# Kernel tuning notes

Measured on AMD Instinct MI355X. Metric: run time of the kernel, lower is better.

The kernel has to match this reference:

```python
import jax, jax.numpy as jnp
import numpy as np

B, T, C = 2, 2048, 1024
N_HEAD = 16
HEAD_DIM = C // N_HEAD


def setup_inputs() -> dict:
    key = jax.random.key(0)
    k1, k2, k3 = jax.random.split(key, 3)
    x = jax.random.normal(k1, (B, T, C), dtype=jnp.float32)
    # weights stored as [in, out]; torch Linear computes x @ W.T with weight [out, in]
    W_qkv = jax.random.normal(k2, (C, 3 * C), dtype=jnp.float32) * (1.0 / np.sqrt(C))
    W_proj = jax.random.normal(k3, (C, C), dtype=jnp.float32) * (1.0 / np.sqrt(C))
    return {"x": x, "W_qkv": W_qkv, "W_proj": W_proj}


def reference(x, W_qkv, W_proj):
    Bb, Tt, Cc = x.shape
    qkv = x @ W_qkv                                # [B,T,3C]
    q, k, v = jnp.split(qkv, 3, axis=2)
    # [B,T,H,D] -> [B,H,T,D]
    q = q.reshape(Bb, Tt, N_HEAD, HEAD_DIM).transpose(0, 2, 1, 3)
    k = k.reshape(Bb, Tt, N_HEAD, HEAD_DIM).transpose(0, 2, 1, 3)
    v = v.reshape(Bb, Tt, N_HEAD, HEAD_DIM).transpose(0, 2, 1, 3)
    scale = 1.0 / np.sqrt(HEAD_DIM).astype(np.float32)
    att = jnp.einsum('bhqd,bhkd->bhqk', q, k) * scale   # [B,H,T,T]
    causal = jnp.tril(jnp.ones((Tt, Tt), dtype=bool))
    att = jnp.where(causal[None, None], att, -jnp.inf)
    att = jax.nn.softmax(att, axis=-1)
    y = jnp.einsum('bhqk,bhkd->bhqd', att, v)           # [B,H,T,D]
    y = y.transpose(0, 2, 1, 3).reshape(Bb, Tt, Cc)
    return y @ W_proj
```

## Files before the change

### kernel.cpp

```cpp
#include <hip/hip_runtime.h>
#include <hip/hip_bf16.h>
#include <math.h>


typedef __bf16 bf16_t;
typedef __bf16 bf16x4 __attribute__((ext_vector_type(4)));
typedef __bf16 bf16x8 __attribute__((ext_vector_type(8)));
typedef float  f32x4  __attribute__((ext_vector_type(4)));

#define MFMA16(a, b, c) __builtin_amdgcn_mfma_f32_16x16x32_bf16((a), (b), (c), 0, 0, 0)

#define Bn 2
#define Tn 2048
#define Cn 1024
#define Hn 16
#define Dn 64
#define C3 3072
#define Mn 4096
#define QKW 2048
#define NEG_BIG (-1e30f)
#define SCL2 0.18033688011112042f
#define M2   17.31234049066756f

__device__ __forceinline__ void gload_lds16(const void* g, void* l) {
    __builtin_amdgcn_global_load_lds(
        (const __attribute__((address_space(1))) unsigned int*)g,
        (__attribute__((address_space(3))) unsigned int*)l, 16, 0, 0);
}

__device__ __forceinline__ bf16x8 cat44(bf16x4 a, bf16x4 b) {
    bf16x8 r;
    r[0] = a[0]; r[1] = a[1]; r[2] = a[2]; r[3] = a[3];
    r[4] = b[0]; r[5] = b[1]; r[6] = b[2]; r[7] = b[3];
    return r;
}

__global__ __launch_bounds__(256) void transpose_cvt(const float* __restrict__ in,
                                                     bf16_t* __restrict__ out,
                                                     int K, int N) {
    __shared__ float tile[32][33];
    int n0 = blockIdx.x * 32, k0 = blockIdx.y * 32;
    int tx = threadIdx.x, ty = threadIdx.y;
#pragma unroll
    for (int i = 0; i < 32; i += 8)
        tile[ty + i][tx] = in[(size_t)(k0 + ty + i) * N + n0 + tx];
    __syncthreads();
#pragma unroll
    for (int i = 0; i < 32; i += 8)
        out[(size_t)(n0 + ty + i) * K + k0 + tx] = (bf16_t)tile[tx][ty + i];
}

__global__ __launch_bounds__(256) void cvt_bf16(const float* __restrict__ in,
                                                bf16_t* __restrict__ out) {
    size_t i = ((size_t)blockIdx.x * 256 + threadIdx.x) * 8;
    f32x4 a = *(const f32x4*)(in + i);
    f32x4 b = *(const f32x4*)(in + i + 4);
    bf16x8 r;
    r[0] = (bf16_t)a[0]; r[1] = (bf16_t)a[1]; r[2] = (bf16_t)a[2]; r[3] = (bf16_t)a[3];
    r[4] = (bf16_t)b[0]; r[5] = (bf16_t)b[1]; r[6] = (bf16_t)b[2]; r[7] = (bf16_t)b[3];
    *(bf16x8*)(out + i) = r;
}

template <typename AT, typename CT, int MODE>
__global__ __launch_bounds__(256) void gemm_m97(const AT* __restrict__ A, int lda,
                                                const bf16_t* __restrict__ BT,
                                                CT* __restrict__ Cout, int ldc, int Kd,
                                                bf16_t* __restrict__ qk,
                                                bf16_t* __restrict__ vT) {
    constexpr bool AF32 = (sizeof(AT) == 4);
    __shared__ AT     As[128 * 32];
    __shared__ bf16_t Bs[128 * 32];

    const int tid = threadIdx.x;
    const int w = tid >> 6, lane = tid & 63;
    const int l16 = lane & 15, quad = lane >> 4;
    const int wm = w & 1, wn = w >> 1;
    const int n0 = blockIdx.x * 128;
    const int m0 = blockIdx.y * 128;

    f32x4 zero = {0.f, 0.f, 0.f, 0.f};
    f32x4 acc[4][4];
#pragma unroll
    for (int mb = 0; mb < 4; mb++)
#pragma unroll
        for (int nb = 0; nb < 4; nb++) acc[mb][nb] = zero;

    for (int k = 0; k < Kd; k += 32) {
        __syncthreads();
        if (AF32) {
#pragma unroll
            for (int j = 0; j < 4; j++) {
                int seg = w * 4 + j;
                int r = seg * 8 + (lane >> 3);
                int cc = (lane & 7) ^ (r & 7);
                const float* g = (const float*)A + (size_t)(m0 + r) * lda + k + cc * 4;
                gload_lds16(g, (char*)As + seg * 1024);
            }
        } else {
#pragma unroll
            for (int j = 0; j < 2; j++) {
                int seg = w * 2 + j;
                int r = seg * 16 + (lane >> 2);
                int cc = (lane & 3) ^ (r & 3);
                const bf16_t* g = (const bf16_t*)A + (size_t)(m0 + r) * lda + k + cc * 8;
                gload_lds16(g, (char*)As + seg * 1024);
            }
        }
#pragma unroll
        for (int j = 0; j < 2; j++) {
            int seg = w * 2 + j;
            int r = seg * 16 + (lane >> 2);
            int cc = (lane & 3) ^ (r & 3);
            const bf16_t* g = BT + (size_t)(n0 + r) * Kd + k + cc * 8;
            gload_lds16(g, (char*)Bs + seg * 1024);
        }
        __syncthreads();

        bf16x8 af[4], bf[4];
#pragma unroll
        for (int mb = 0; mb < 4; mb++) {
            int r = wm * 64 + mb * 16 + l16;
            if (AF32) {
                f32x4 x0 = *(const f32x4*)((const char*)As + (r * 8 + ((quad * 2) ^ (r & 7))) * 16);
                f32x4 x1 = *(const f32x4*)((const char*)As + (r * 8 + ((quad * 2 + 1) ^ (r & 7))) * 16);
                bf16x8 t;
                t[0] = (bf16_t)x0[0]; t[1] = (bf16_t)x0[1]; t[2] = (bf16_t)x0[2]; t[3] = (bf16_t)x0[3];
                t[4] = (bf16_t)x1[0]; t[5] = (bf16_t)x1[1]; t[6] = (bf16_t)x1[2]; t[7] = (bf16_t)x1[3];
                af[mb] = t;
            } else {
                af[mb] = *(const bf16x8*)((const char*)As + (r * 4 + (quad ^ (r & 3))) * 16);
            }
        }
#pragma unroll
        for (int nb = 0; nb < 4; nb++) {
            int r = wn * 64 + nb * 16 + l16;
            bf[nb] = *(const bf16x8*)((const char*)Bs + (r * 4 + (quad ^ (r & 3))) * 16);
        }
#pragma unroll
        for (int mb = 0; mb < 4; mb++)
#pragma unroll
            for (int nb = 0; nb < 4; nb++)
                acc[mb][nb] = MFMA16(af[mb], bf[nb], acc[mb][nb]);
    }

#pragma unroll
    for (int mb = 0; mb < 4; mb++)
#pragma unroll
        for (int nb = 0; nb < 4; nb++) {
            const int col = n0 + wn * 64 + nb * 16 + l16;
            const int row0 = m0 + wm * 64 + mb * 16 + quad * 4;
            if (MODE == 0) {
#pragma unroll
                for (int rr = 0; rr < 4; rr++)
                    Cout[(size_t)(row0 + rr) * ldc + col] = (CT)acc[mb][nb][rr];
            } else {
                if (col < 2048) {
#pragma unroll
                    for (int rr = 0; rr < 4; rr++)
                        qk[(size_t)(row0 + rr) * QKW + col] = (bf16_t)acc[mb][nb][rr];
                } else {
                    int hcol = col - 2048;
                    int bb = row0 >> 11, t0 = row0 & 2047;
                    bf16x4 pv;
#pragma unroll
                    for (int rr = 0; rr < 4; rr++) pv[rr] = (bf16_t)acc[mb][nb][rr];
                    *(bf16x4*)(vT + ((size_t)(bb * 1024 + hcol)) * Tn + t0) = pv;
                }
            }
        }
}

__global__ __launch_bounds__(256) void gemm_s(const bf16_t* __restrict__ A, int lda,
                                              const bf16_t* __restrict__ BT,
                                              float* __restrict__ Cout, int ldc, int Kd) {
    __shared__ bf16_t As[64 * 32];
    __shared__ bf16_t Bs[128 * 32];

    const int tid = threadIdx.x;
    const int w = tid >> 6, lane = tid & 63;
    const int l16 = lane & 15, quad = lane >> 4;
    const int wm = w & 1, wn = w >> 1;
    const int n0 = blockIdx.x * 128;
    const int m0 = blockIdx.y * 64;

    f32x4 zero = {0.f, 0.f, 0.f, 0.f};
    f32x4 acc[2][4];
#pragma unroll
    for (int mb = 0; mb < 2; mb++)
#pragma unroll
        for (int nb = 0; nb < 4; nb++) acc[mb][nb] = zero;

    for (int k = 0; k < Kd; k += 32) {
        __syncthreads();
        {
            int r = w * 16 + (lane >> 2);
            int cc = (lane & 3) ^ (r & 3);
            const bf16_t* g = A + (size_t)(m0 + r) * lda + k + cc * 8;
            gload_lds16(g, (char*)As + w * 1024);
        }
#pragma unroll
        for (int j = 0; j < 2; j++) {
            int seg = w * 2 + j;
            int r = seg * 16 + (lane >> 2);
            int cc = (lane & 3) ^ (r & 3);
            const bf16_t* g = BT + (size_t)(n0 + r) * Kd + k + cc * 8;
            gload_lds16(g, (char*)Bs + seg * 1024);
        }
        __syncthreads();

        bf16x8 af[2], bf[4];
#pragma unroll
        for (int mb = 0; mb < 2; mb++) {
            int r = wm * 32 + mb * 16 + l16;
            af[mb] = *(const bf16x8*)((const char*)As + (r * 4 + (quad ^ (r & 3))) * 16);
        }
#pragma unroll
        for (int nb = 0; nb < 4; nb++) {
            int r = wn * 64 + nb * 16 + l16;
            bf[nb] = *(const bf16x8*)((const char*)Bs + (r * 4 + (quad ^ (r & 3))) * 16);
        }
#pragma unroll
        for (int mb = 0; mb < 2; mb++)
#pragma unroll
            for (int nb = 0; nb < 4; nb++)
                acc[mb][nb] = MFMA16(af[mb], bf[nb], acc[mb][nb]);
    }

#pragma unroll
    for (int mb = 0; mb < 2; mb++)
#pragma unroll
        for (int nb = 0; nb < 4; nb++) {
            const int col = n0 + wn * 64 + nb * 16 + l16;
            const int row0 = m0 + wm * 32 + mb * 16 + quad * 4;
#pragma unroll
            for (int rr = 0; rr < 4; rr++)
                Cout[(size_t)(row0 + rr) * ldc + col] = acc[mb][nb][rr];
        }
}

__global__ __launch_bounds__(256) void attn_kernel(bf16_t* __restrict__ qk,
                                                   const bf16_t* __restrict__ vT) {
    const int id = blockIdx.x;
    const int bh = id & 31;
    const int pr = id >> 5;
    const int b = bh >> 4, h = bh & 15;
    const int tA = pr;
    const int tB = 31 - pr;
    const int tmax = tB;

    const int tid = threadIdx.x;
    const int wave = tid >> 6, lane = tid & 63;
    const int l16 = lane & 15, quad = lane >> 4;

    __shared__ bf16_t Kb[2][64 * 64];
    __shared__ bf16_t Vb[2][64 * 64];

    bf16_t* qbase = qk + (size_t)b * Tn * QKW + h * Dn;
    const bf16_t* kbase = qk + (size_t)b * Tn * QKW + Cn + h * Dn;
    const bf16_t* vbase = vT + (size_t)(b * 1024 + h * Dn) * Tn;

    const int qA = tA * 64 + wave * 16;
    const int qB = tB * 64 + wave * 16;

    bf16x8 qfA[2], qfB[2];
#pragma unroll
    for (int ks = 0; ks < 2; ks++) {
        qfA[ks] = *(const bf16x8*)(qbase + (size_t)(qA + l16) * QKW + ks * 32 + quad * 8);
        qfB[ks] = *(const bf16x8*)(qbase + (size_t)(qB + l16) * QKW + ks * 32 + quad * 8);
    }

    bf16x8 ones;
#pragma unroll
    for (int j = 0; j < 8; j++) ones[j] = (bf16_t)1.0f;

    f32x4 zero = {0.f, 0.f, 0.f, 0.f};
    f32x4 oA[4], oB[4];
    f32x4 olA, olB;
#pragma unroll
    for (int i = 0; i < 4; i++) { oA[i] = zero; oB[i] = zero; }
    olA = zero; olB = zero;

    const int r8 = lane >> 3;
    const int cc = (lane & 7) ^ r8;
    auto STAGE = [&](int t, int pg) {
        const int key0 = t * 64;
#pragma unroll
        for (int j = 0; j < 2; j++) {
            int seg = wave * 2 + j;
            gload_lds16(kbase + (size_t)(key0 + seg * 8 + r8) * QKW + cc * 8,
                        (char*)&Kb[pg][0] + seg * 1024);
            gload_lds16(vbase + (size_t)(seg * 8 + r8) * Tn + key0 + cc * 8,
                        (char*)&Vb[pg][0] + seg * 1024);
        }
    };

    STAGE(0, 0);
    int cur = 0;

    for (int t = 0; t <= tmax; ++t) {
        __syncthreads();
        if (t < tmax) STAGE(t + 1, cur ^ 1);

        const bool shp = (t <= tA);
        const char* Kc = (const char*)&Kb[cur][0];
        const char* Vc = (const char*)&Vb[cur][0];

        bf16x8 kf[2][4];
#pragma unroll
        for (int ks = 0; ks < 2; ks++)
#pragma unroll
            for (int nbk = 0; nbk < 4; nbk++) {
                int R = nbk * 16 + l16;
                kf[ks][nbk] = *(const bf16x8*)(Kc + R * 128 +
                                               (((ks * 4 + quad) ^ (R & 7)) << 4));
            }

        bf16x4 pkA[4], pkB[4];

        {
            f32x4 s[4];
#pragma unroll
            for (int nbk = 0; nbk < 4; nbk++) s[nbk] = zero;
            __builtin_amdgcn_s_setprio(1);
#pragma unroll
            for (int nbk = 0; nbk < 4; nbk++) {
                s[nbk] = MFMA16(kf[0][nbk], qfB[0], s[nbk]);
                s[nbk] = MFMA16(kf[1][nbk], qfB[1], s[nbk]);
            }
            __builtin_amdgcn_s_setprio(0);
            if (t == tB) {
                int q = qB + l16;
#pragma unroll
                for (int nbk = 0; nbk < 4; nbk++)
#pragma unroll
                    for (int r = 0; r < 4; r++) {
                        int key = t * 64 + nbk * 16 + quad * 4 + r;
                        if (key > q) s[nbk][r] = NEG_BIG;
                    }
            }
#pragma unroll
            for (int nbk = 0; nbk < 4; nbk++)
#pragma unroll
                for (int r = 0; r < 4; r++)
                    pkB[nbk][r] = (bf16_t)__builtin_exp2f(__builtin_fmaf(s[nbk][r], SCL2, -M2));
        }

        if (shp) {
            f32x4 s[4];
#pragma unroll
            for (int nbk = 0; nbk < 4; nbk++) s[nbk] = zero;
            __builtin_amdgcn_s_setprio(1);
#pragma unroll
            for (int nbk = 0; nbk < 4; nbk++) {
                s[nbk] = MFMA16(kf[0][nbk], qfA[0], s[nbk]);
                s[nbk] = MFMA16(kf[1][nbk], qfA[1], s[nbk]);
            }
            __builtin_amdgcn_s_setprio(0);
            if (t == tA) {
                int q = qA + l16;
#pragma unroll
                for (int nbk = 0; nbk < 4; nbk++)
#pragma unroll
                    for (int r = 0; r < 4; r++) {
                        int key = t * 64 + nbk * 16 + quad * 4 + r;
                        if (key > q) s[nbk][r] = NEG_BIG;
                    }
            }
#pragma unroll
            for (int nbk = 0; nbk < 4; nbk++)
#pragma unroll
                for (int r = 0; r < 4; r++)
                    pkA[nbk][r] = (bf16_t)__builtin_exp2f(__builtin_fmaf(s[nbk][r], SCL2, -M2));
        } else {
#pragma unroll
            for (int nbk = 0; nbk < 4; nbk++)
#pragma unroll
                for (int r = 0; r < 4; r++) pkA[nbk][r] = (bf16_t)0.0f;
        }

        const int gl = quad >> 1, sub = (quad & 1) * 8;
        __builtin_amdgcn_s_setprio(1);
#pragma unroll
        for (int ks = 0; ks < 2; ks++) {
            bf16x8 pfB_ = cat44(pkB[2 * ks], pkB[2 * ks + 1]);
            bf16x8 pfA_ = cat44(pkA[2 * ks], pkA[2 * ks + 1]);
#pragma unroll
            for (int nbd = 0; nbd < 4; nbd++) {
                int R = nbd * 16 + l16, r7 = R & 7;
                const char* row = Vc + R * 128;
                bf16x4 lo = *(const bf16x4*)(row + (((ks * 4 + gl) ^ r7) << 4) + sub);
                bf16x4 hi = *(const bf16x4*)(row + (((ks * 4 + 2 + gl) ^ r7) << 4) + sub);
                bf16x8 vf = cat44(lo, hi);
                oB[nbd] = MFMA16(pfB_, vf, oB[nbd]);
                if (shp) oA[nbd] = MFMA16(pfA_, vf, oA[nbd]);
            }
            olB = MFMA16(pfB_, ones, olB);
            if (shp) olA = MFMA16(pfA_, ones, olA);
        }
        __builtin_amdgcn_s_setprio(0);

        cur ^= 1;
    }

#pragma unroll
    for (int nbd = 0; nbd < 4; nbd++)
#pragma unroll
        for (int r = 0; r < 4; r++) {
            int ta = qA + quad * 4 + r;
            int tb = qB + quad * 4 + r;
            qbase[(size_t)ta * QKW + nbd * 16 + l16] = (bf16_t)(oA[nbd][r] / olA[r]);
            qbase[(size_t)tb * QKW + nbd * 16 + l16] = (bf16_t)(oB[nbd][r] / olB[r]);
        }
}

extern "C" void kernel_launch(void* const* d_in, const int* in_sizes, int n_in,
                              void* d_out, int out_size, void* d_ws, size_t ws_size,
                              hipStream_t stream) {
    const float* x     = (const float*)d_in[0];
    const float* Wqkv  = (const float*)d_in[1];
    const float* Wproj = (const float*)d_in[2];
    float* out = (float*)d_out;

    bf16_t* qk     = (bf16_t*)d_ws;
    bf16_t* vT     = qk + (size_t)Mn * QKW;
    bf16_t* wqkvT  = vT + (size_t)QKW * Tn;
    bf16_t* wprojT = wqkvT + (size_t)C3 * Cn;
    bf16_t* xb     = wprojT + (size_t)Cn * Cn;

    const size_t NEED_XB = ((size_t)Mn * QKW + (size_t)QKW * Tn + (size_t)C3 * Cn +
                            (size_t)Cn * Cn + (size_t)Mn * Cn) * sizeof(bf16_t);

    transpose_cvt<<<dim3(C3 / 32, Cn / 32), dim3(32, 8), 0, stream>>>(Wqkv, wqkvT, Cn, C3);
    transpose_cvt<<<dim3(Cn / 32, Cn / 32), dim3(32, 8), 0, stream>>>(Wproj, wprojT, Cn, Cn);

    if (ws_size >= NEED_XB) {
        cvt_bf16<<<dim3((Mn * Cn) / 2048), 256, 0, stream>>>(x, xb);
        gemm_m97<bf16_t, bf16_t, 1><<<dim3(C3 / 128, Mn / 128), 256, 0, stream>>>(
            xb, Cn, wqkvT, (bf16_t*)nullptr, 0, Cn, qk, vT);
    } else {
        gemm_m97<float, bf16_t, 1><<<dim3(C3 / 128, Mn / 128), 256, 0, stream>>>(
            x, Cn, wqkvT, (bf16_t*)nullptr, 0, Cn, qk, vT);
    }
    attn_kernel<<<dim3(512), 256, 0, stream>>>(qk, vT);
    gemm_s<<<dim3(Cn / 128, Mn / 64), 256, 0, stream>>>(qk, QKW, wprojT, out, Cn, Cn);
}
```

Measured before the change: 192.9 us.

## Split attention key loop across two wave groups and merge partial sums

Doubles the attention block to 512 threads and gives each half of the waves alternating key tiles, with separate double-buffered K/V LDS per half. At the end, half 1 writes its partial output and row-sum accumulators to LDS and half 0 adds them before normalizing and storing. This works because softmax here uses a fixed max offset, so partials add directly. The aim is to halve the sequential key loop per block and expose more parallelism per CU, at the cost of doubled LDS, an extra reduction step and a higher register-pressure launch bound.

```diff
diff --git a/kernel.cpp b/kernel.cpp
--- a/kernel.cpp
+++ b/kernel.cpp
@@ -238,8 +238,8 @@
         }
 }
 
-__global__ __launch_bounds__(256) void attn_kernel(bf16_t* __restrict__ qk,
-                                                   const bf16_t* __restrict__ vT) {
+__global__ __launch_bounds__(512, 4) void attn_kernel(bf16_t* __restrict__ qk,
+                                                      const bf16_t* __restrict__ vT) {
     const int id = blockIdx.x;
     const int bh = id & 31;
     const int pr = id >> 5;
@@ -250,17 +250,18 @@
 
     const int tid = threadIdx.x;
     const int wave = tid >> 6, lane = tid & 63;
+    const int half = wave >> 2, wv = wave & 3;
     const int l16 = lane & 15, quad = lane >> 4;
 
-    __shared__ bf16_t Kb[2][64 * 64];
-    __shared__ bf16_t Vb[2][64 * 64];
+    __shared__ __align__(16) bf16_t Kb[2][2][64 * 64];
+    __shared__ __align__(16) bf16_t Vb[2][2][64 * 64];
 
     bf16_t* qbase = qk + (size_t)b * Tn * QKW + h * Dn;
     const bf16_t* kbase = qk + (size_t)b * Tn * QKW + Cn + h * Dn;
     const bf16_t* vbase = vT + (size_t)(b * 1024 + h * Dn) * Tn;
 
-    const int qA = tA * 64 + wave * 16;
-    const int qB = tB * 64 + wave * 16;
+    const int qA = tA * 64 + wv * 16;
+    const int qB = tB * 64 + wv * 16;
 
     bf16x8 qfA[2], qfB[2];
 #pragma unroll
@@ -286,131 +287,158 @@
         const int key0 = t * 64;
 #pragma unroll
         for (int j = 0; j < 2; j++) {
-            int seg = wave * 2 + j;
+            int seg = wv * 2 + j;
             gload_lds16(kbase + (size_t)(key0 + seg * 8 + r8) * QKW + cc * 8,
-                        (char*)&Kb[pg][0] + seg * 1024);
+                        (char*)&Kb[half][pg][0] + seg * 1024);
             gload_lds16(vbase + (size_t)(seg * 8 + r8) * Tn + key0 + cc * 8,
-                        (char*)&Vb[pg][0] + seg * 1024);
+                        (char*)&Vb[half][pg][0] + seg * 1024);
         }
     };
 
-    STAGE(0, 0);
+    STAGE(half, 0);
     int cur = 0;
 
-    for (int t = 0; t <= tmax; ++t) {
+    const int S = (tmax + 2) >> 1;
+    for (int s = 0; s < S; ++s) {
         __syncthreads();
-        if (t < tmax) STAGE(t + 1, cur ^ 1);
-
-        const bool shp = (t <= tA);
-        const char* Kc = (const char*)&Kb[cur][0];
-        const char* Vc = (const char*)&Vb[cur][0];
-
-        bf16x8 kf[2][4];
-#pragma unroll
-        for (int ks = 0; ks < 2; ks++)
-#pragma unroll
-            for (int nbk = 0; nbk < 4; nbk++) {
-                int R = nbk * 16 + l16;
-                kf[ks][nbk] = *(const bf16x8*)(Kc + R * 128 +
-                                               (((ks * 4 + quad) ^ (R & 7)) << 4));
-            }
-
-        bf16x4 pkA[4], pkB[4];
-
-        {
-            f32x4 s[4];
-#pragma unroll
-            for (int nbk = 0; nbk < 4; nbk++) s[nbk] = zero;
+        const int t = 2 * s + half;
+        if (t + 2 <= tmax) STAGE(t + 2, cur ^ 1);
+
+        if (t <= tmax) {
+            const bool shp = (t <= tA);
+            const char* Kc = (const char*)&Kb[half][cur][0];
+            const char* Vc = (const char*)&Vb[half][cur][0];
+
+            bf16x8 kf[2][4];
+#pragma unroll
+            for (int ks = 0; ks < 2; ks++)
+#pragma unroll
+                for (int nbk = 0; nbk < 4; nbk++) {
+                    int R = nbk * 16 + l16;
+                    kf[ks][nbk] = *(const bf16x8*)(Kc + R * 128 +
+                                                   (((ks * 4 + quad) ^ (R & 7)) << 4));
+                }
+
+            bf16x4 pkA[4], pkB[4];
+
+            {
+                f32x4 sx[4];
+#pragma unroll
+                for (int nbk = 0; nbk < 4; nbk++) sx[nbk] = zero;
+                __builtin_amdgcn_s_setprio(1);
+#pragma unroll
+                for (int nbk = 0; nbk < 4; nbk++) {
+                    sx[nbk] = MFMA16(kf[0][nbk], qfB[0], sx[nbk]);
+                    sx[nbk] = MFMA16(kf[1][nbk], qfB[1], sx[nbk]);
+                }
+                __builtin_amdgcn_s_setprio(0);
+                if (t == tB) {
+                    int q = qB + l16;
+#pragma unroll
+                    for (int nbk = 0; nbk < 4; nbk++)
+#pragma unroll
+                        for (int r = 0; r < 4; r++) {
+                            int key = t * 64 + nbk * 16 + quad * 4 + r;
+                            if (key > q) sx[nbk][r] = NEG_BIG;
+                        }
+                }
+#pragma unroll
+                for (int nbk = 0; nbk < 4; nbk++)
+#pragma unroll
+                    for (int r = 0; r < 4; r++)
+                        pkB[nbk][r] = (bf16_t)__builtin_exp2f(__builtin_fmaf(sx[nbk][r], SCL2, -M2));
+            }
+
+            if (shp) {
+                f32x4 sx[4];
+#pragma unroll
+                for (int nbk = 0; nbk < 4; nbk++) sx[nbk] = zero;
+                __builtin_amdgcn_s_setprio(1);
+#pragma unroll
+                for (int nbk = 0; nbk < 4; nbk++) {
+                    sx[nbk] = MFMA16(kf[0][nbk], qfA[0], sx[nbk]);
+                    sx[nbk] = MFMA16(kf[1][nbk], qfA[1], sx[nbk]);
+                }
+                __builtin_amdgcn_s_setprio(0);
+                if (t == tA) {
+                    int q = qA + l16;
+#pragma unroll
+                    for (int nbk = 0; nbk < 4; nbk++)
+#pragma unroll
+                        for (int r = 0; r < 4; r++) {
+                            int key = t * 64 + nbk * 16 + quad * 4 + r;
+                            if (key > q) sx[nbk][r] = NEG_BIG;
+                        }
+                }
+#pragma unroll
+                for (int nbk = 0; nbk < 4; nbk++)
+#pragma unroll
+                    for (int r = 0; r < 4; r++)
+                        pkA[nbk][r] = (bf16_t)__builtin_exp2f(__builtin_fmaf(sx[nbk][r], SCL2, -M2));
+            } else {
+#pragma unroll
+                for (int nbk = 0; nbk < 4; nbk++)
+#pragma unroll
+                    for (int r = 0; r < 4; r++) pkA[nbk][r] = (bf16_t)0.0f;
+            }
+
+            const int gl = quad >> 1, sub = (quad & 1) * 8;
             __builtin_amdgcn_s_setprio(1);
 #pragma unroll
-            for (int nbk = 0; nbk < 4; nbk++) {
-                s[nbk] = MFMA16(kf[0][nbk], qfB[0], s[nbk]);
-                s[nbk] = MFMA16(kf[1][nbk], qfB[1], s[nbk]);
+            for (int ks = 0; ks < 2; ks++) {
+                bf16x8 pfB_ = cat44(pkB[2 * ks], pkB[2 * ks + 1]);
+                bf16x8 pfA_ = cat44(pkA[2 * ks], pkA[2 * ks + 1]);
+#pragma unroll
+                for (int nbd = 0; nbd < 4; nbd++) {
+                    int R = nbd * 16 + l16, r7 = R & 7;
+                    const char* row = Vc + R * 128;
+                    bf16x4 lo = *(const bf16x4*)(row + (((ks * 4 + gl) ^ r7) << 4) + sub);
+                    bf16x4 hi = *(const bf16x4*)(row + (((ks * 4 + 2 + gl) ^ r7) << 4) + sub);
+                    bf16x8 vf = cat44(lo, hi);
+                    oB[nbd] = MFMA16(pfB_, vf, oB[nbd]);
+                    if (shp) oA[nbd] = MFMA16(pfA_, vf, oA[nbd]);
+                }
+                olB = MFMA16(pfB_, ones, olB);
+                if (shp) olA = MFMA16(pfA_, ones, olA);
             }
             __builtin_amdgcn_s_setprio(0);
-            if (t == tB) {
-                int q = qB + l16;
-#pragma unroll
-                for (int nbk = 0; nbk < 4; nbk++)
-#pragma unroll
-                    for (int r = 0; r < 4; r++) {
-                        int key = t * 64 + nbk * 16 + quad * 4 + r;
-                        if (key > q) s[nbk][r] = NEG_BIG;
-                    }
-            }
-#pragma unroll
-            for (int nbk = 0; nbk < 4; nbk++)
-#pragma unroll
-                for (int r = 0; r < 4; r++)
-                    pkB[nbk][r] = (bf16_t)__builtin_exp2f(__builtin_fmaf(s[nbk][r], SCL2, -M2));
-        }
-
-        if (shp) {
-            f32x4 s[4];
-#pragma unroll
-            for (int nbk = 0; nbk < 4; nbk++) s[nbk] = zero;
-            __builtin_amdgcn_s_setprio(1);
-#pragma unroll
-            for (int nbk = 0; nbk < 4; nbk++) {
-                s[nbk] = MFMA16(kf[0][nbk], qfA[0], s[nbk]);
-                s[nbk] = MFMA16(kf[1][nbk], qfA[1], s[nbk]);
-            }
-            __builtin_amdgcn_s_setprio(0);
-            if (t == tA) {
-                int q = qA + l16;
-#pragma unroll
-                for (int nbk = 0; nbk < 4; nbk++)
-#pragma unroll
-                    for (int r = 0; r < 4; r++) {
-                        int key = t * 64 + nbk * 16 + quad * 4 + r;
-                        if (key > q) s[nbk][r] = NEG_BIG;
-                    }
-            }
-#pragma unroll
-            for (int nbk = 0; nbk < 4; nbk++)
-#pragma unroll
-                for (int r = 0; r < 4; r++)
-                    pkA[nbk][r] = (bf16_t)__builtin_exp2f(__builtin_fmaf(s[nbk][r], SCL2, -M2));
-        } else {
-#pragma unroll
-            for (int nbk = 0; nbk < 4; nbk++)
-#pragma unroll
-                for (int r = 0; r < 4; r++) pkA[nbk][r] = (bf16_t)0.0f;
-        }
-
-        const int gl = quad >> 1, sub = (quad & 1) * 8;
-        __builtin_amdgcn_s_setprio(1);
-#pragma unroll
-        for (int ks = 0; ks < 2; ks++) {
-            bf16x8 pfB_ = cat44(pkB[2 * ks], pkB[2 * ks + 1]);
-            bf16x8 pfA_ = cat44(pkA[2 * ks], pkA[2 * ks + 1]);
-#pragma unroll
-            for (int nbd = 0; nbd < 4; nbd++) {
-                int R = nbd * 16 + l16, r7 = R & 7;
-                const char* row = Vc + R * 128;
-                bf16x4 lo = *(const bf16x4*)(row + (((ks * 4 + gl) ^ r7) << 4) + sub);
-                bf16x4 hi = *(const bf16x4*)(row + (((ks * 4 + 2 + gl) ^ r7) << 4) + sub);
-                bf16x8 vf = cat44(lo, hi);
-                oB[nbd] = MFMA16(pfB_, vf, oB[nbd]);
-                if (shp) oA[nbd] = MFMA16(pfA_, vf, oA[nbd]);
-            }
-            olB = MFMA16(pfB_, ones, olB);
-            if (shp) olA = MFMA16(pfA_, ones, olA);
-        }
-        __builtin_amdgcn_s_setprio(0);
+        }
 
         cur ^= 1;
     }
 
-#pragma unroll
-    for (int nbd = 0; nbd < 4; nbd++)
-#pragma unroll
-        for (int r = 0; r < 4; r++) {
-            int ta = qA + quad * 4 + r;
-            int tb = qB + quad * 4 + r;
-            qbase[(size_t)ta * QKW + nbd * 16 + l16] = (bf16_t)(oA[nbd][r] / olA[r]);
-            qbase[(size_t)tb * QKW + nbd * 16 + l16] = (bf16_t)(oB[nbd][r] / olB[r]);
-        }
+    __syncthreads();
+    float* cbo = (float*)&Kb[0][0][0];
+    float* cbl = (float*)&Vb[0][0][0];
+    if (half == 1) {
+#pragma unroll
+        for (int nbd = 0; nbd < 4; nbd++) {
+            *(f32x4*)(cbo + ((0 * 4 + nbd) * 4 + wv) * 256 + lane * 4) = oA[nbd];
+            *(f32x4*)(cbo + ((1 * 4 + nbd) * 4 + wv) * 256 + lane * 4) = oB[nbd];
+        }
+        *(f32x4*)(cbl + (0 * 4 + wv) * 256 + lane * 4) = olA;
+        *(f32x4*)(cbl + (1 * 4 + wv) * 256 + lane * 4) = olB;
+    }
+    __syncthreads();
+    if (half == 0) {
+#pragma unroll
+        for (int nbd = 0; nbd < 4; nbd++) {
+            oA[nbd] += *(const f32x4*)(cbo + ((0 * 4 + nbd) * 4 + wv) * 256 + lane * 4);
+            oB[nbd] += *(const f32x4*)(cbo + ((1 * 4 + nbd) * 4 + wv) * 256 + lane * 4);
+        }
+        olA += *(const f32x4*)(cbl + (0 * 4 + wv) * 256 + lane * 4);
+        olB += *(const f32x4*)(cbl + (1 * 4 + wv) * 256 + lane * 4);
+
+#pragma unroll
+        for (int nbd = 0; nbd < 4; nbd++)
+#pragma unroll
+            for (int r = 0; r < 4; r++) {
+                int ta = qA + quad * 4 + r;
+                int tb = qB + quad * 4 + r;
+                qbase[(size_t)ta * QKW + nbd * 16 + l16] = (bf16_t)(oA[nbd][r] / olA[r]);
+                qbase[(size_t)tb * QKW + nbd * 16 + l16] = (bf16_t)(oB[nbd][r] / olB[r]);
+            }
+    }
 }
 
 extern "C" void kernel_launch(void* const* d_in, const int* in_sizes, int n_in,
@@ -441,6 +469,6 @@
         gemm_m97<float, bf16_t, 1><<<dim3(C3 / 128, Mn / 128), 256, 0, stream>>>(
             x, Cn, wqkvT, (bf16_t*)nullptr, 0, Cn, qk, vT);
     }
-    attn_kernel<<<dim3(512), 256, 0, stream>>>(qk, vT);
+    attn_kernel<<<dim3(512), 512, 0, stream>>>(qk, vT);
     gemm_s<<<dim3(Cn / 128, Mn / 64), 256, 0, stream>>>(qk, QKW, wprojT, out, Cn, Cn);
 }
```

Result: no change. 196.7 us (+2.0%).

## Triple-buffer attention K/V loads and write V row-major then transpose separately

Applied to the files above, without the earlier changes.

The attention kernel goes from double to triple buffering of K/V tiles in LDS. It prefetches two tiles ahead and replaces __syncthreads with an explicit vmcnt wait plus s_barrier, so global loads overlap more of the compute. The QKV GEMM epilogue now writes V row-major with coalesced stores instead of the scattered transposed bf16x4 stores. A separate transpose kernel then builds vT into the xb buffer. This adds an extra kernel launch and a full V round trip, and raises LDS use per block.

```diff
diff --git a/kernel.cpp b/kernel.cpp
--- a/kernel.cpp
+++ b/kernel.cpp
@@ -50,6 +50,24 @@
         out[(size_t)(n0 + ty + i) * K + k0 + tx] = (bf16_t)tile[tx][ty + i];
 }
 
+__global__ __launch_bounds__(256) void transpose_v(const bf16_t* __restrict__ in,
+                                                   bf16_t* __restrict__ out) {
+    __shared__ bf16_t tile[32][34];
+    int c0 = blockIdx.x * 32;
+    int t0 = blockIdx.y * 32;
+    int b  = blockIdx.z;
+    const bf16_t* ib = in  + (size_t)b * Tn * Cn;
+    bf16_t* ob       = out + (size_t)b * Cn * Tn;
+    int tx = threadIdx.x, ty = threadIdx.y;
+#pragma unroll
+    for (int i = 0; i < 32; i += 8)
+        tile[ty + i][tx] = ib[(size_t)(t0 + ty + i) * Cn + c0 + tx];
+    __syncthreads();
+#pragma unroll
+    for (int i = 0; i < 32; i += 8)
+        ob[(size_t)(c0 + ty + i) * Tn + t0 + tx] = tile[tx][ty + i];
+}
+
 __global__ __launch_bounds__(256) void cvt_bf16(const float* __restrict__ in,
                                                 bf16_t* __restrict__ out) {
     size_t i = ((size_t)blockIdx.x * 256 + threadIdx.x) * 8;
@@ -158,6 +176,11 @@
 #pragma unroll
                     for (int rr = 0; rr < 4; rr++)
                         qk[(size_t)(row0 + rr) * QKW + col] = (bf16_t)acc[mb][nb][rr];
+                } else if (MODE == 2) {
+                    int hcol = col - 2048;
+#pragma unroll
+                    for (int rr = 0; rr < 4; rr++)
+                        vT[(size_t)(row0 + rr) * Cn + hcol] = (bf16_t)acc[mb][nb][rr];
                 } else {
                     int hcol = col - 2048;
                     int bb = row0 >> 11, t0 = row0 & 2047;
@@ -252,8 +275,8 @@
     const int wave = tid >> 6, lane = tid & 63;
     const int l16 = lane & 15, quad = lane >> 4;
 
-    __shared__ bf16_t Kb[2][64 * 64];
-    __shared__ bf16_t Vb[2][64 * 64];
+    __shared__ __align__(16) bf16_t Kb[3][64 * 64];
+    __shared__ __align__(16) bf16_t Vb[3][64 * 64];
 
     bf16_t* qbase = qk + (size_t)b * Tn * QKW + h * Dn;
     const bf16_t* kbase = qk + (size_t)b * Tn * QKW + Cn + h * Dn;
@@ -295,11 +318,19 @@
     };
 
     STAGE(0, 0);
+    STAGE(1, 1);
     int cur = 0;
 
     for (int t = 0; t <= tmax; ++t) {
-        __syncthreads();
-        if (t < tmax) STAGE(t + 1, cur ^ 1);
+        asm volatile("s_waitcnt vmcnt(4)" ::: "memory");
+        __builtin_amdgcn_sched_barrier(0);
+        __builtin_amdgcn_s_barrier();
+        __builtin_amdgcn_sched_barrier(0);
+        if (t + 2 <= tmax) {
+            int st = cur + 2; if (st >= 3) st -= 3;
+            STAGE(t + 2, st);
+        }
+        __builtin_amdgcn_sched_barrier(0);
 
         const bool shp = (t <= tA);
         const char* Kc = (const char*)&Kb[cur][0];
@@ -318,14 +349,14 @@
         bf16x4 pkA[4], pkB[4];
 
         {
-            f32x4 s[4];
-#pragma unroll
-            for (int nbk = 0; nbk < 4; nbk++) s[nbk] = zero;
+            f32x4 sx[4];
+#pragma unroll
+            for (int nbk = 0; nbk < 4; nbk++) sx[nbk] = zero;
             __builtin_amdgcn_s_setprio(1);
 #pragma unroll
             for (int nbk = 0; nbk < 4; nbk++) {
-                s[nbk] = MFMA16(kf[0][nbk], qfB[0], s[nbk]);
-                s[nbk] = MFMA16(kf[1][nbk], qfB[1], s[nbk]);
+                sx[nbk] = MFMA16(kf[0][nbk], qfB[0], sx[nbk]);
+                sx[nbk] = MFMA16(kf[1][nbk], qfB[1], sx[nbk]);
             }
             __builtin_amdgcn_s_setprio(0);
             if (t == tB) {
@@ -335,25 +366,25 @@
 #pragma unroll
                     for (int r = 0; r < 4; r++) {
                         int key = t * 64 + nbk * 16 + quad * 4 + r;
-                        if (key > q) s[nbk][r] = NEG_BIG;
+                        if (key > q) sx[nbk][r] = NEG_BIG;
                     }
             }
 #pragma unroll
             for (int nbk = 0; nbk < 4; nbk++)
 #pragma unroll
                 for (int r = 0; r < 4; r++)
-                    pkB[nbk][r] = (bf16_t)__builtin_exp2f(__builtin_fmaf(s[nbk][r], SCL2, -M2));
+                    pkB[nbk][r] = (bf16_t)__builtin_exp2f(__builtin_fmaf(sx[nbk][r], SCL2, -M2));
         }
 
         if (shp) {
-            f32x4 s[4];
-#pragma unroll
-            for (int nbk = 0; nbk < 4; nbk++) s[nbk] = zero;
+            f32x4 sx[4];
+#pragma unroll
+            for (int nbk = 0; nbk < 4; nbk++) sx[nbk] = zero;
             __builtin_amdgcn_s_setprio(1);
 #pragma unroll
             for (int nbk = 0; nbk < 4; nbk++) {
-                s[nbk] = MFMA16(kf[0][nbk], qfA[0], s[nbk]);
-                s[nbk] = MFMA16(kf[1][nbk], qfA[1], s[nbk]);
+                sx[nbk] = MFMA16(kf[0][nbk], qfA[0], sx[nbk]);
+                sx[nbk] = MFMA16(kf[1][nbk], qfA[1], sx[nbk]);
             }
             __builtin_amdgcn_s_setprio(0);
             if (t == tA) {
@@ -363,14 +394,14 @@
 #pragma unroll
                     for (int r = 0; r < 4; r++) {
                         int key = t * 64 + nbk * 16 + quad * 4 + r;
-                        if (key > q) s[nbk][r] = NEG_BIG;
+                        if (key > q) sx[nbk][r] = NEG_BIG;
                     }
             }
 #pragma unroll
             for (int nbk = 0; nbk < 4; nbk++)
 #pragma unroll
                 for (int r = 0; r < 4; r++)
-                    pkA[nbk][r] = (bf16_t)__builtin_exp2f(__builtin_fmaf(s[nbk][r], SCL2, -M2));
+                    pkA[nbk][r] = (bf16_t)__builtin_exp2f(__builtin_fmaf(sx[nbk][r], SCL2, -M2));
         } else {
 #pragma unroll
             for (int nbk = 0; nbk < 4; nbk++)
@@ -399,7 +430,7 @@
         }
         __builtin_amdgcn_s_setprio(0);
 
-        cur ^= 1;
+        cur = cur + 1; if (cur >= 3) cur -= 3;
     }
 
 #pragma unroll
@@ -422,8 +453,8 @@
     float* out = (float*)d_out;
 
     bf16_t* qk     = (bf16_t*)d_ws;
-    bf16_t* vT     = qk + (size_t)Mn * QKW;
-    bf16_t* wqkvT  = vT + (size_t)QKW * Tn;
+    bf16_t* vslot  = qk + (size_t)Mn * QKW;
+    bf16_t* wqkvT  = vslot + (size_t)QKW * Tn;
     bf16_t* wprojT = wqkvT + (size_t)C3 * Cn;
     bf16_t* xb     = wprojT + (size_t)Cn * Cn;
 
@@ -435,12 +466,14 @@
 
     if (ws_size >= NEED_XB) {
         cvt_bf16<<<dim3((Mn * Cn) / 2048), 256, 0, stream>>>(x, xb);
-        gemm_m97<bf16_t, bf16_t, 1><<<dim3(C3 / 128, Mn / 128), 256, 0, stream>>>(
-            xb, Cn, wqkvT, (bf16_t*)nullptr, 0, Cn, qk, vT);
+        gemm_m97<bf16_t, bf16_t, 2><<<dim3(C3 / 128, Mn / 128), 256, 0, stream>>>(
+            xb, Cn, wqkvT, (bf16_t*)nullptr, 0, Cn, qk, vslot);
+        transpose_v<<<dim3(Cn / 32, Tn / 32, Bn), dim3(32, 8), 0, stream>>>(vslot, xb);
+        attn_kernel<<<dim3(512), 256, 0, stream>>>(qk, xb);
     } else {
         gemm_m97<float, bf16_t, 1><<<dim3(C3 / 128, Mn / 128), 256, 0, stream>>>(
-            x, Cn, wqkvT, (bf16_t*)nullptr, 0, Cn, qk, vT);
+            x, Cn, wqkvT, (bf16_t*)nullptr, 0, Cn, qk, vslot);
+        attn_kernel<<<dim3(512), 256, 0, stream>>>(qk, vslot);
     }
-    attn_kernel<<<dim3(512), 256, 0, stream>>>(qk, vT);
     gemm_s<<<dim3(Cn / 128, Mn / 64), 256, 0, stream>>>(qk, QKW, wprojT, out, Cn, Cn);
 }
```

Measured after the change: 197.9 us. 1.03x slower.
